# Kernel tuning notes

Measured on AMD Instinct MI355X. Metric: run time of the kernel, lower is better.

## Reference

```python
import jax, jax.numpy as jnp
import numpy as np

NUM_HEADS = 8

def setup_inputs() -> dict:
    key = jax.random.key(0)
    k1, k2, k3, k4, k5 = jax.random.split(key, 5)
    B, N, C = 4, 2048, 512
    x = jax.random.normal(k1, (B, N, C), dtype=jnp.float32)
    s = 1.0 / np.sqrt(C)
    qkv_w = jax.random.uniform(k2, (3 * C, C), dtype=jnp.float32, minval=-s, maxval=s)
    qkv_b = jax.random.uniform(k3, (3 * C,), dtype=jnp.float32, minval=-s, maxval=s)
    proj_w = jax.random.uniform(k4, (C, C), dtype=jnp.float32, minval=-s, maxval=s)
    proj_b = jax.random.uniform(k5, (C,), dtype=jnp.float32, minval=-s, maxval=s)
    return {"x": x, "qkv_w": qkv_w, "qkv_b": qkv_b, "proj_w": proj_w, "proj_b": proj_b}

def reference(x, qkv_w, qkv_b, proj_w, proj_b):
    B, N, C = x.shape
    H = NUM_HEADS
    D = C // H
    scale = D ** -0.5
    # qkv: [B,N,3C] -> [3,B,H,N,D]
    qkv = (jnp.einsum('bnc,oc->bno', x, qkv_w) + qkv_b)
    qkv = qkv.reshape(B, N, 3, H, D).transpose(2, 0, 3, 1, 4)
    q, k, v = qkv[0], qkv[1], qkv[2]
    attn = jnp.einsum('bhnd,bhmd->bhnm', q, k) * scale  # [B,H,N,N]
    attn = jax.nn.softmax(attn, axis=-1)
    out = jnp.einsum('bhnm,bhmd->bhnd', attn, v)  # [B,H,N,D]
    out = out.transpose(0, 2, 1, 3).reshape(B, N, C)
    return jnp.einsum('bnc,oc->bno', out, proj_w) + proj_b
```

## Files before the change

### kernel.cpp

```cpp
#include <hip/hip_runtime.h>
#include <stdint.h>


typedef short bf16x8 __attribute__((ext_vector_type(8)));
typedef float f32x4  __attribute__((ext_vector_type(4)));
typedef float f32x16 __attribute__((ext_vector_type(16)));
typedef unsigned int u32x4 __attribute__((ext_vector_type(4)));

__device__ __forceinline__ unsigned short f2bf(float f) {
    unsigned int u = __builtin_bit_cast(unsigned int, f);
    u += 0x7fffu + ((u >> 16) & 1u);
    return (unsigned short)(u >> 16);
}
__device__ __forceinline__ unsigned int pk2(float a, float b) {
    return (unsigned int)f2bf(a) | ((unsigned int)f2bf(b) << 16);
}
__device__ __forceinline__ float fexp2(float x) {
    return __builtin_amdgcn_exp2f(x);
}
__device__ __forceinline__ bf16x8 ld8_f32(const float* __restrict__ p) {
    float4 f0 = *(const float4*)p;
    float4 f1 = *(const float4*)(p + 4);
    u32x4 u = {pk2(f0.x, f0.y), pk2(f0.z, f0.w), pk2(f1.x, f1.y), pk2(f1.z, f1.w)};
    return __builtin_bit_cast(bf16x8, u);
}
__device__ __forceinline__ void async16(const void* g, void* l) {
    __builtin_amdgcn_global_load_lds(
        (const __attribute__((address_space(1))) unsigned int*)g,
        (__attribute__((address_space(3))) unsigned int*)l,
        16, 0, 0);
}

#define MFMA16(a, b, c) __builtin_amdgcn_mfma_f32_16x16x32_bf16((a), (b), (c), 0, 0, 0)
#define MFMA32(a, b, c) __builtin_amdgcn_mfma_f32_32x32x16_bf16((a), (b), (c), 0, 0, 0)

__global__ void cvt_bf16(const float* __restrict__ x,
                         const float* __restrict__ w,
                         unsigned short* __restrict__ xb,
                         unsigned short* __restrict__ wb)
{
    const int G = 524288 + 98304;
    for (int idx = blockIdx.x * 256 + threadIdx.x; idx < G; idx += gridDim.x * 256) {
        if (idx < 524288)
            *(bf16x8*)(xb + (size_t)idx * 8) = ld8_f32(x + (size_t)idx * 8);
        else {
            int j = idx - 524288;
            *(bf16x8*)(wb + (size_t)j * 8) = ld8_f32(w + (size_t)j * 8);
        }
    }
}

template <int MODE>
__global__ __launch_bounds__(256, 2)
void gemm_bt(const unsigned short* __restrict__ A,
             const void* __restrict__ Bp,
             const float* __restrict__ bias,
             unsigned short* __restrict__ out0,
             unsigned short* __restrict__ out1,
             unsigned short* __restrict__ out2,
             float* __restrict__ outf,
             int K, int N)
{
    __shared__ unsigned short sA[128 * 32];
    __shared__ unsigned short sB[128 * 32];

    const int tid  = threadIdx.x;
    const int wave = tid >> 6, lane = tid & 63;
    const int l = lane & 15, q16 = lane >> 4;
    const int wm = wave >> 1, wn = wave & 1;
    const int m0 = blockIdx.y * 128;
    const int n0 = blockIdx.x * 128;

    f32x4 acc[4][4];
#pragma unroll
    for (int i = 0; i < 4; ++i)
#pragma unroll
        for (int j = 0; j < 4; ++j)
            acc[i][j] = (f32x4){0.f, 0.f, 0.f, 0.f};

    for (int k0 = 0; k0 < K; k0 += 32) {
#pragma unroll
        for (int call = 0; call < 2; ++call) {
            int L = call * 256 + tid;
            int r = L >> 2, c = L & 3;
            async16(A + (size_t)(m0 + r) * K + k0 + c * 8, sA + L * 8);
            if (MODE == 0)
                async16((const unsigned short*)Bp + (size_t)(n0 + r) * K + k0 + c * 8,
                        sB + L * 8);
            else
                *(bf16x8*)(sB + L * 8) =
                    ld8_f32((const float*)Bp + (size_t)(n0 + r) * K + k0 + c * 8);
        }
        __syncthreads();

        bf16x8 af[4], bfr[4];
#pragma unroll
        for (int i = 0; i < 4; ++i) {
            int row = wm * 64 + i * 16 + l;
            af[i] = *(const bf16x8*)(sA + (row * 4 + q16) * 8);
        }
#pragma unroll
        for (int j = 0; j < 4; ++j) {
            int row = wn * 64 + j * 16 + l;
            bfr[j] = *(const bf16x8*)(sB + (row * 4 + q16) * 8);
        }
#pragma unroll
        for (int i = 0; i < 4; ++i)
#pragma unroll
            for (int j = 0; j < 4; ++j)
                acc[i][j] = MFMA16(af[i], bfr[j], acc[i][j]);
        __syncthreads();
    }

    const float lscale = 0.18033688f;
#pragma unroll
    for (int i = 0; i < 4; ++i) {
#pragma unroll
        for (int j = 0; j < 4; ++j) {
            int col = n0 + wn * 64 + j * 16 + l;
            float bv = bias[col];
#pragma unroll
            for (int r = 0; r < 4; ++r) {
                int row = m0 + wm * 64 + i * 16 + q16 * 4 + r;
                float val = acc[i][j][r] + bv;
                if (MODE == 0) {
                    int which = col >> 9;
                    int h = (col >> 6) & 7, d = col & 63;
                    int b = row >> 11, n = row & 2047;
                    if (which == 0)
                        out0[(size_t)(((b * 8 + h) * 2048) + n) * 64 + d] = f2bf(val * lscale);
                    else if (which == 1)
                        out1[(size_t)(((b * 8 + h) * 2048) + n) * 64 + d] = f2bf(val);
                    else
                        out2[(size_t)(((b * 8 + h) * 64) + d) * 2048 + n] = f2bf(val);
                } else {
                    outf[(size_t)row * N + col] = val;
                }
            }
        }
    }
}

__global__ __launch_bounds__(256, 2)
void attn_fused(const unsigned short* __restrict__ Q,
                const unsigned short* __restrict__ Km,
                const unsigned short* __restrict__ Vt,
                unsigned short* __restrict__ O)
{
    __shared__ unsigned short sK[2][64 * 72];
    __shared__ unsigned short sVt[2][64 * 72];

    const int tid  = threadIdx.x;
    const int wave = tid >> 6, lane = tid & 63;
    const int l31 = lane & 31, h = lane >> 5;
    const int bh = blockIdx.y;
    const int n0 = blockIdx.x * 128;
    const int q0 = n0 + wave * 32;

    const int r0 = tid >> 3, c0 = tid & 7, r1 = r0 + 32;
    const size_t kbase = (size_t)bh * 2048 * 64;
    const size_t vbase = (size_t)bh * 64 * 2048;

    bf16x8 qf[4];
#pragma unroll
    for (int ks = 0; ks < 4; ++ks)
        qf[ks] = *(const bf16x8*)(Q + (size_t)(bh * 2048 + q0 + l31) * 64 + ks * 16 + h * 8);

    f32x16 oacc[2];
#pragma unroll
    for (int dt = 0; dt < 2; ++dt)
#pragma unroll
        for (int e = 0; e < 16; ++e) oacc[dt][e] = 0.f;
    float m_run = -1e30f, l_run = 0.f;

    bf16x8 kr0 = *(const bf16x8*)(Km + kbase + (size_t)r0 * 64 + c0 * 8);
    bf16x8 kr1 = *(const bf16x8*)(Km + kbase + (size_t)r1 * 64 + c0 * 8);
    bf16x8 vr0 = *(const bf16x8*)(Vt + vbase + (size_t)r0 * 2048 + c0 * 8);
    bf16x8 vr1 = *(const bf16x8*)(Vt + vbase + (size_t)r1 * 2048 + c0 * 8);
    *(bf16x8*)(&sK[0][r0 * 72 + c0 * 8])  = kr0;
    *(bf16x8*)(&sK[0][r1 * 72 + c0 * 8])  = kr1;
    *(bf16x8*)(&sVt[0][r0 * 72 + c0 * 8]) = vr0;
    *(bf16x8*)(&sVt[0][r1 * 72 + c0 * 8]) = vr1;
    __syncthreads();

    for (int it = 0; it < 32; ++it) {
        const int cur = it & 1;
        if (it < 31) {
            int kv = (it + 1) * 64;
            kr0 = *(const bf16x8*)(Km + kbase + (size_t)(kv + r0) * 64 + c0 * 8);
            kr1 = *(const bf16x8*)(Km + kbase + (size_t)(kv + r1) * 64 + c0 * 8);
            vr0 = *(const bf16x8*)(Vt + vbase + (size_t)r0 * 2048 + kv + c0 * 8);
            vr1 = *(const bf16x8*)(Vt + vbase + (size_t)r1 * 2048 + kv + c0 * 8);
        }

        f32x16 sacc[2];
#pragma unroll
        for (int mt = 0; mt < 2; ++mt) {
#pragma unroll
            for (int e = 0; e < 16; ++e) sacc[mt][e] = 0.f;
            const unsigned short* kp = &sK[cur][(mt * 32 + l31) * 72];
#pragma unroll
            for (int ks = 0; ks < 4; ++ks) {
                bf16x8 kf = *(const bf16x8*)(kp + (ks * 2 + h) * 8);
                sacc[mt] = MFMA32(kf, qf[ks], sacc[mt]);
            }
        }

        float mx = -1e30f;
#pragma unroll
        for (int mt = 0; mt < 2; ++mt)
#pragma unroll
            for (int e = 0; e < 16; ++e) mx = fmaxf(mx, sacc[mt][e]);
        mx = fmaxf(mx, __shfl_xor(mx, 32));
        float mn = fmaxf(m_run, mx);
        if (__any((mn > m_run) ? 1 : 0)) {
            float a = fexp2(m_run - mn);
            m_run = mn;
            l_run *= a;
#pragma unroll
            for (int dt = 0; dt < 2; ++dt)
#pragma unroll
                for (int e = 0; e < 16; ++e) oacc[dt][e] *= a;
        }
        float rs = 0.f;
        unsigned int pk[2][4][2];
#pragma unroll
        for (int mt = 0; mt < 2; ++mt)
#pragma unroll
            for (int g = 0; g < 4; ++g) {
                unsigned int u0 = __builtin_bit_cast(unsigned int, fexp2(sacc[mt][4 * g + 0] - mn));
                unsigned int u1 = __builtin_bit_cast(unsigned int, fexp2(sacc[mt][4 * g + 1] - mn));
                unsigned int u2 = __builtin_bit_cast(unsigned int, fexp2(sacc[mt][4 * g + 2] - mn));
                unsigned int u3 = __builtin_bit_cast(unsigned int, fexp2(sacc[mt][4 * g + 3] - mn));
                unsigned int t0 = u0 & 0xffff0000u, t1 = u1 & 0xffff0000u;
                unsigned int t2 = u2 & 0xffff0000u, t3 = u3 & 0xffff0000u;
                rs += (__builtin_bit_cast(float, t0) + __builtin_bit_cast(float, t1))
                    + (__builtin_bit_cast(float, t2) + __builtin_bit_cast(float, t3));
                pk[mt][g][0] = (u0 >> 16) | t1;
                pk[mt][g][1] = (u2 >> 16) | t3;
            }
        rs += __shfl_xor(rs, 32);
        l_run += rs;

#pragma unroll
        for (int mt = 0; mt < 2; ++mt) {
#pragma unroll
            for (int ks2 = 0; ks2 < 2; ++ks2) {
                unsigned int send0 = h ? pk[mt][2 * ks2][0] : pk[mt][2 * ks2 + 1][0];
                unsigned int send1 = h ? pk[mt][2 * ks2][1] : pk[mt][2 * ks2 + 1][1];
                unsigned int rcv0 = __shfl_xor(send0, 32);
                unsigned int rcv1 = __shfl_xor(send1, 32);
                unsigned int own0 = h ? pk[mt][2 * ks2 + 1][0] : pk[mt][2 * ks2][0];
                unsigned int own1 = h ? pk[mt][2 * ks2 + 1][1] : pk[mt][2 * ks2][1];
                u32x4 bu;
                bu[0] = h ? rcv0 : own0;
                bu[1] = h ? rcv1 : own1;
                bu[2] = h ? own0 : rcv0;
                bu[3] = h ? own1 : rcv1;
                bf16x8 bfrag = __builtin_bit_cast(bf16x8, bu);
#pragma unroll
                for (int dt = 0; dt < 2; ++dt) {
                    bf16x8 vf = *(const bf16x8*)(&sVt[cur][(dt * 32 + l31) * 72
                                                           + (mt * 4 + ks2 * 2 + h) * 8]);
                    oacc[dt] = MFMA32(vf, bfrag, oacc[dt]);
                }
            }
        }

        if (it < 31) {
            const int nxt = cur ^ 1;
            *(bf16x8*)(&sK[nxt][r0 * 72 + c0 * 8])  = kr0;
            *(bf16x8*)(&sK[nxt][r1 * 72 + c0 * 8])  = kr1;
            *(bf16x8*)(&sVt[nxt][r0 * 72 + c0 * 8]) = vr0;
            *(bf16x8*)(&sVt[nxt][r1 * 72 + c0 * 8]) = vr1;
        }
        __syncthreads();
    }

    const int b = bh >> 3, hh = bh & 7;
    float inv = 1.f / fmaxf(l_run, 1e-20f);
    unsigned short* obase = O + ((size_t)(b * 2048 + q0 + l31)) * 512 + hh * 64;
#pragma unroll
    for (int dt = 0; dt < 2; ++dt)
#pragma unroll
        for (int g = 0; g < 4; ++g) {
            int d = dt * 32 + 8 * g + 4 * h;
            unsigned int w0 = pk2(oacc[dt][4 * g + 0] * inv, oacc[dt][4 * g + 1] * inv);
            unsigned int w1 = pk2(oacc[dt][4 * g + 2] * inv, oacc[dt][4 * g + 3] * inv);
            uint2 w = {w0, w1};
            *(uint2*)(obase + d) = w;
        }
}

extern "C" void kernel_launch(void* const* d_in, const int* in_sizes, int n_in,
                              void* d_out, int out_size, void* d_ws, size_t ws_size,
                              hipStream_t stream)
{
    const float* x      = (const float*)d_in[0];
    const float* qkv_w  = (const float*)d_in[1];
    const float* qkv_b  = (const float*)d_in[2];
    const float* proj_w = (const float*)d_in[3];
    const float* proj_b = (const float*)d_in[4];

    const size_t PER = 4u * 8u * 2048u * 64u;
    unsigned short* q_ws  = (unsigned short*)d_ws;
    unsigned short* k_ws  = q_ws  + PER;
    unsigned short* vt_ws = k_ws  + PER;
    unsigned short* ao_ws = vt_ws + PER;

    unsigned short* xb = (unsigned short*)d_out;
    unsigned short* wb = xb + PER;

    cvt_bf16<<<dim3(640), 256, 0, stream>>>(x, qkv_w, xb, wb);
    gemm_bt<0><<<dim3(12, 64), 256, 0, stream>>>(
        xb, wb, qkv_b, q_ws, k_ws, vt_ws, nullptr, 512, 1536);
    attn_fused<<<dim3(16, 32), 256, 0, stream>>>(q_ws, k_ws, vt_ws, ao_ws);
    gemm_bt<1><<<dim3(4, 64), 256, 0, stream>>>(
        ao_ws, proj_w, proj_b, nullptr, nullptr, nullptr, (float*)d_out, 512, 512);
}
```

Baseline: 182.0 us.

## Use async LDS staging with XOR swizzle and 128-key tiles in attention

The attention kernel now stages K and V tiles straight into shared memory with async 16-byte copies instead of going through registers. It swaps the padded layout for an XOR-swizzled one to avoid bank conflicts, and doubles the KV tile to 128 keys so there are half as many iterations and barriers. A separate kernel converts proj_w to bf16 into the now-free K workspace, so the projection GEMM can also use async loads for B. The cost is doubled LDS per block, which may reduce occupancy, plus one extra kernel launch.

```diff
diff --git a/kernel.cpp b/kernel.cpp
--- a/kernel.cpp
+++ b/kernel.cpp
@@ -49,11 +49,16 @@
         }
     }
 }
+__global__ void cvt_w2(const float* __restrict__ w, unsigned short* __restrict__ wb)
+{
+    int idx = blockIdx.x * 256 + threadIdx.x;
+    *(bf16x8*)(wb + (size_t)idx * 8) = ld8_f32(w + (size_t)idx * 8);
+}
 
 template <int MODE>
 __global__ __launch_bounds__(256, 2)
 void gemm_bt(const unsigned short* __restrict__ A,
-             const void* __restrict__ Bp,
+             const unsigned short* __restrict__ B,
              const float* __restrict__ bias,
              unsigned short* __restrict__ out0,
              unsigned short* __restrict__ out1,
@@ -84,12 +89,7 @@
             int L = call * 256 + tid;
             int r = L >> 2, c = L & 3;
             async16(A + (size_t)(m0 + r) * K + k0 + c * 8, sA + L * 8);
-            if (MODE == 0)
-                async16((const unsigned short*)Bp + (size_t)(n0 + r) * K + k0 + c * 8,
-                        sB + L * 8);
-            else
-                *(bf16x8*)(sB + L * 8) =
-                    ld8_f32((const float*)Bp + (size_t)(n0 + r) * K + k0 + c * 8);
+            async16(B + (size_t)(n0 + r) * K + k0 + c * 8, sB + L * 8);
         }
         __syncthreads();
 
@@ -147,8 +147,8 @@
                 const unsigned short* __restrict__ Vt,
                 unsigned short* __restrict__ O)
 {
-    __shared__ unsigned short sK[2][64 * 72];
-    __shared__ unsigned short sVt[2][64 * 72];
+    __shared__ unsigned short sK[2][128 * 64];
+    __shared__ unsigned short sVt[2][64 * 128];
 
     const int tid  = threadIdx.x;
     const int wave = tid >> 6, lane = tid & 63;
@@ -157,7 +157,6 @@
     const int n0 = blockIdx.x * 128;
     const int q0 = n0 + wave * 32;
 
-    const int r0 = tid >> 3, c0 = tid & 7, r1 = r0 + 32;
     const size_t kbase = (size_t)bh * 2048 * 64;
     const size_t vbase = (size_t)bh * 64 * 2048;
 
@@ -173,42 +172,41 @@
         for (int e = 0; e < 16; ++e) oacc[dt][e] = 0.f;
     float m_run = -1e30f, l_run = 0.f;
 
-    bf16x8 kr0 = *(const bf16x8*)(Km + kbase + (size_t)r0 * 64 + c0 * 8);
-    bf16x8 kr1 = *(const bf16x8*)(Km + kbase + (size_t)r1 * 64 + c0 * 8);
-    bf16x8 vr0 = *(const bf16x8*)(Vt + vbase + (size_t)r0 * 2048 + c0 * 8);
-    bf16x8 vr1 = *(const bf16x8*)(Vt + vbase + (size_t)r1 * 2048 + c0 * 8);
-    *(bf16x8*)(&sK[0][r0 * 72 + c0 * 8])  = kr0;
-    *(bf16x8*)(&sK[0][r1 * 72 + c0 * 8])  = kr1;
-    *(bf16x8*)(&sVt[0][r0 * 72 + c0 * 8]) = vr0;
-    *(bf16x8*)(&sVt[0][r1 * 72 + c0 * 8]) = vr1;
+    auto stage = [&](int buf, int kv) {
+#pragma unroll
+        for (int call = 0; call < 4; ++call) {
+            int s = wave * 256 + call * 64 + lane;
+            int rk = s >> 3, ck = (s & 7) ^ (rk & 7);
+            async16(Km + kbase + (size_t)(kv + rk) * 64 + ck * 8, &sK[buf][s * 8]);
+            int rv = s >> 4, cv = (s & 15) ^ (rv & 7);
+            async16(Vt + vbase + (size_t)rv * 2048 + kv + cv * 8, &sVt[buf][s * 8]);
+        }
+    };
+
+    stage(0, 0);
     __syncthreads();
 
-    for (int it = 0; it < 32; ++it) {
+    for (int it = 0; it < 16; ++it) {
         const int cur = it & 1;
-        if (it < 31) {
-            int kv = (it + 1) * 64;
-            kr0 = *(const bf16x8*)(Km + kbase + (size_t)(kv + r0) * 64 + c0 * 8);
-            kr1 = *(const bf16x8*)(Km + kbase + (size_t)(kv + r1) * 64 + c0 * 8);
-            vr0 = *(const bf16x8*)(Vt + vbase + (size_t)r0 * 2048 + kv + c0 * 8);
-            vr1 = *(const bf16x8*)(Vt + vbase + (size_t)r1 * 2048 + kv + c0 * 8);
-        }
-
-        f32x16 sacc[2];
-#pragma unroll
-        for (int mt = 0; mt < 2; ++mt) {
+        if (it < 15) stage(cur ^ 1, (it + 1) * 128);
+
+        f32x16 sacc[4];
+#pragma unroll
+        for (int mt = 0; mt < 4; ++mt) {
 #pragma unroll
             for (int e = 0; e < 16; ++e) sacc[mt][e] = 0.f;
-            const unsigned short* kp = &sK[cur][(mt * 32 + l31) * 72];
+            const int rk = mt * 32 + l31;
 #pragma unroll
             for (int ks = 0; ks < 4; ++ks) {
-                bf16x8 kf = *(const bf16x8*)(kp + (ks * 2 + h) * 8);
+                int c = ks * 2 + h;
+                bf16x8 kf = *(const bf16x8*)(&sK[cur][(rk * 8 + (c ^ (rk & 7))) * 8]);
                 sacc[mt] = MFMA32(kf, qf[ks], sacc[mt]);
             }
         }
 
         float mx = -1e30f;
 #pragma unroll
-        for (int mt = 0; mt < 2; ++mt)
+        for (int mt = 0; mt < 4; ++mt)
 #pragma unroll
             for (int e = 0; e < 16; ++e) mx = fmaxf(mx, sacc[mt][e]);
         mx = fmaxf(mx, __shfl_xor(mx, 32));
@@ -223,9 +221,9 @@
                 for (int e = 0; e < 16; ++e) oacc[dt][e] *= a;
         }
         float rs = 0.f;
-        unsigned int pk[2][4][2];
-#pragma unroll
-        for (int mt = 0; mt < 2; ++mt)
+        unsigned int pk[4][4][2];
+#pragma unroll
+        for (int mt = 0; mt < 4; ++mt)
 #pragma unroll
             for (int g = 0; g < 4; ++g) {
                 unsigned int u0 = __builtin_bit_cast(unsigned int, fexp2(sacc[mt][4 * g + 0] - mn));
@@ -243,7 +241,7 @@
         l_run += rs;
 
 #pragma unroll
-        for (int mt = 0; mt < 2; ++mt) {
+        for (int mt = 0; mt < 4; ++mt) {
 #pragma unroll
             for (int ks2 = 0; ks2 < 2; ++ks2) {
                 unsigned int send0 = h ? pk[mt][2 * ks2][0] : pk[mt][2 * ks2 + 1][0];
@@ -258,21 +256,14 @@
                 bu[2] = h ? own0 : rcv0;
                 bu[3] = h ? own1 : rcv1;
                 bf16x8 bfrag = __builtin_bit_cast(bf16x8, bu);
+                int c = mt * 4 + ks2 * 2 + h;
 #pragma unroll
                 for (int dt = 0; dt < 2; ++dt) {
-                    bf16x8 vf = *(const bf16x8*)(&sVt[cur][(dt * 32 + l31) * 72
-                                                           + (mt * 4 + ks2 * 2 + h) * 8]);
+                    int rv = dt * 32 + l31;
+                    bf16x8 vf = *(const bf16x8*)(&sVt[cur][(rv * 16 + (c ^ (rv & 7))) * 8]);
                     oacc[dt] = MFMA32(vf, bfrag, oacc[dt]);
                 }
             }
-        }
-
-        if (it < 31) {
-            const int nxt = cur ^ 1;
-            *(bf16x8*)(&sK[nxt][r0 * 72 + c0 * 8])  = kr0;
-            *(bf16x8*)(&sK[nxt][r1 * 72 + c0 * 8])  = kr1;
-            *(bf16x8*)(&sVt[nxt][r0 * 72 + c0 * 8]) = vr0;
-            *(bf16x8*)(&sVt[nxt][r1 * 72 + c0 * 8]) = vr1;
         }
         __syncthreads();
     }
@@ -315,6 +306,7 @@
     gemm_bt<0><<<dim3(12, 64), 256, 0, stream>>>(
         xb, wb, qkv_b, q_ws, k_ws, vt_ws, nullptr, 512, 1536);
     attn_fused<<<dim3(16, 32), 256, 0, stream>>>(q_ws, k_ws, vt_ws, ao_ws);
+    cvt_w2<<<dim3(128), 256, 0, stream>>>(proj_w, k_ws);
     gemm_bt<1><<<dim3(4, 64), 256, 0, stream>>>(
-        ao_ws, proj_w, proj_b, nullptr, nullptr, nullptr, (float*)d_out, 512, 512);
-}
+        ao_ws, k_ws, proj_b, nullptr, nullptr, nullptr, (float*)d_out, 512, 512);
+}
```

Measured after the change: 176.6 us. 3.0% less time.
